# Performance work log

Measured on AMD Instinct MI355X. Metric: run time of the kernel, lower is better.

## Reference

```python
import jax, jax.numpy as jnp
import numpy as np

N, E, G = 20000, 640000, 64
D_IN, H, C, D_OUT = 256, 4, 64, 32
HC = H * C


def gat_layer(x, W, a_src, a_dst, b, src, dst, n_nodes, heads, ch):
    # x: [N, F_in], W: [F_in, H*C]
    h = (x @ W).reshape(n_nodes, heads, ch)          # [N,H,C]
    es = jnp.einsum('nhc,hc->nh', h, a_src)          # [N,H]
    ed = jnp.einsum('nhc,hc->nh', h, a_dst)
    e = jax.nn.leaky_relu(es[src] + ed[dst], 0.2)    # [Etot,H]
    m = jax.ops.segment_max(e, dst, num_segments=n_nodes)
    m = jnp.where(jnp.isfinite(m), m, 0.0)
    ex = jnp.exp(e - m[dst])
    denom = jax.ops.segment_sum(ex, dst, num_segments=n_nodes)
    alpha = ex / jnp.maximum(denom[dst], 1e-16)      # softmax over in-edges per dst
    out = jax.ops.segment_sum(alpha[:, :, None] * h[src], dst, num_segments=n_nodes)
    return out.reshape(n_nodes, heads * ch) + b


def setup_inputs() -> dict:
    key = jax.random.key(0)
    ks = jax.random.split(key, 14)
    g1 = 1.0 / np.sqrt(D_IN)
    g2 = 1.0 / np.sqrt(HC)
    inp = {
        'x': jax.random.normal(ks[0], (N, D_IN), jnp.float32),
        'edge_index': jax.random.randint(ks[1], (2, E), 0, N, jnp.int64 if jax.config.jax_enable_x64 else jnp.int32),
        'batch': jnp.sort(jax.random.randint(ks[2], (N,), 0, G)),
        'W1': jax.random.normal(ks[3], (D_IN, HC), jnp.float32) * g1,
        'a_src1': jax.random.normal(ks[4], (H, C), jnp.float32) * g2,
        'a_dst1': jax.random.normal(ks[5], (H, C), jnp.float32) * g2,
        'b1': jnp.zeros((HC,), jnp.float32),
        'W2': jax.random.normal(ks[6], (HC, HC), jnp.float32) * g2,
        'a_src2': jax.random.normal(ks[7], (H, C), jnp.float32) * g2,
        'a_dst2': jax.random.normal(ks[8], (H, C), jnp.float32) * g2,
        'b2': jnp.zeros((HC,), jnp.float32),
        'Wp': jax.random.normal(ks[9], (HC, D_OUT), jnp.float32) * g2,
        'bp': jnp.zeros((D_OUT,), jnp.float32),
    }
    return inp


def reference(x, edge_index, batch, W1, a_src1, a_dst1, b1, W2, a_src2, a_dst2, b2, Wp, bp):
    # add self-loops (PyG GATConv default)
    loop = jnp.arange(N, dtype=edge_index.dtype)
    src = jnp.concatenate([edge_index[0], loop])
    dst = jnp.concatenate([edge_index[1], loop])
    x1 = jax.nn.relu(gat_layer(x, W1, a_src1, a_dst1, b1, src, dst, N, H, C))
    # dropout p=0.6 is identity in eval mode
    x2 = jax.nn.relu(gat_layer(x1, W2, a_src2, a_dst2, b2, src, dst, N, H, C))
    node_scores = x2 @ Wp + bp                        # [N, D_OUT]
    sums = jax.ops.segment_sum(node_scores, batch, num_segments=G)
    counts = jax.ops.segment_sum(jnp.ones((N,), node_scores.dtype), batch, num_segments=G)
    return sums / jnp.maximum(counts, 1.0)[:, None]   # [G, D_OUT]
```

## Files before the change

### kernel.cpp

```cpp
#include <hip/hip_runtime.h>
#include <hip/hip_bf16.h>
#include <cstdint>

#define NNODES 20000
#define NEDGES 640000
#define ETOT   (NEDGES + NNODES)
#define NGROUP 64
#define HC     256
#define DOUT   32
#define NB     128
#define SL     ((ETOT + NB - 1) / NB)

typedef short bf16x8 __attribute__((ext_vector_type(8)));
typedef short s16x4  __attribute__((ext_vector_type(4)));
typedef float f32x4  __attribute__((ext_vector_type(4)));
typedef float f32x2  __attribute__((ext_vector_type(2)));
typedef int   s32x4  __attribute__((ext_vector_type(4)));
typedef unsigned int u32x4 __attribute__((ext_vector_type(4)));

__device__ __forceinline__ float b2f(__hip_bfloat16 v) { return __bfloat162float(v); }
__device__ __forceinline__ float bs2f(short v) {
    union { unsigned int u; float f; } c; c.u = ((unsigned int)(unsigned short)v) << 16; return c.f;
}
__device__ __forceinline__ short f2bs(float v) {
    __hip_bfloat16 b = __float2bfloat16(v);
    union { __hip_bfloat16 b; short s; } u; u.b = b; return u.s;
}
__device__ __forceinline__ float ldf(const void* __restrict__ p, size_t i, int bf) {
    return bf ? __bfloat162float(((const __hip_bfloat16*)p)[i]) : ((const float*)p)[i];
}
__device__ __forceinline__ int ld_idx(const int* __restrict__ p, size_t i, int f64) {
    return f64 ? p[2 * i] : p[i];
}

__global__ void k_probe(const unsigned int* __restrict__ xw, const int* __restrict__ ei,
                        int* __restrict__ flag) {
    if (threadIdx.x < 64) {
        int l = threadIdx.x;
        int ones = 0, zeros = 0;
#pragma unroll
        for (int r = 0; r < 4; r++) {
            unsigned long long b1 = __ballot((xw[r * 64 + l] >> 14) & 1);
            unsigned long long b2 = __ballot(ei[2 * (r * 64 + l) + 1] == 0);
            ones  += __popcll(b1);
            zeros += __popcll(b2);
        }
        if (l == 0) { flag[1] = (ones < 64) ? 1 : 0; flag[0] = (zeros > 200) ? 1 : 0; }
    }
}

__global__ __launch_bounds__(256) void k_lhist(const int* __restrict__ ei,
                                               int* __restrict__ H,
                                               const int* __restrict__ flag) {
    __shared__ int hl[NNODES];
    int t = threadIdx.x, b = blockIdx.x, f = flag[0];
    for (int i = t; i < NNODES; i += 256) hl[i] = 0;
    __syncthreads();
    int s0 = b * SL, s1 = min(s0 + SL, ETOT);
    for (int i = s0 + t; i < s1; i += 256) {
        int d = (i < NEDGES) ? ld_idx(ei, (size_t)NEDGES + i, f) : (i - NEDGES);
        atomicAdd(&hl[d], 1);
    }
    __syncthreads();
    int* Hb = H + (size_t)b * NNODES;
    for (int i = t; i < NNODES; i += 256) Hb[i] = hl[i];
}

__global__ __launch_bounds__(256) void k_colsum(const int* __restrict__ H,
                                                int* __restrict__ deg) {
    int n = blockIdx.x * 256 + threadIdx.x;
    if (n >= NNODES) return;
    int s = 0;
#pragma unroll 4
    for (int b = 0; b < NB; b++) s += H[(size_t)b * NNODES + n];
    deg[n] = s;
}

__global__ void k_scan(const int* __restrict__ deg, int* __restrict__ off,
                       float* __restrict__ sx, int* __restrict__ cnt) {
    __shared__ int wsum[8];
    int t = threadIdx.x, lane = t & 63, wv = t >> 6;
    for (int i = t; i < NGROUP * HC; i += 512) sx[i] = 0.f;
    if (t < NGROUP) cnt[t] = 0;
    const int CH = ((NNODES + 511) / 512) * 64;
    int base = wv * CH;
    int s = 0;
    for (int i0 = 0; i0 < CH; i0 += 64) {
        int i = base + i0 + lane;
        s += (i < NNODES) ? deg[i] : 0;
    }
#pragma unroll
    for (int o = 1; o < 64; o <<= 1) s += __shfl_xor(s, o);
    if (lane == 0) wsum[wv] = s;
    __syncthreads();
    int run = 0;
    for (int i = 0; i < wv; i++) run += wsum[i];
    for (int i0 = 0; i0 < CH; i0 += 64) {
        int i = base + i0 + lane;
        int v = (i < NNODES) ? deg[i] : 0;
        int sc = v;
#pragma unroll
        for (int o = 1; o < 64; o <<= 1) {
            int u = __shfl_up(sc, o);
            if (lane >= o) sc += u;
        }
        if (i < NNODES) off[i] = run + sc - v;
        run += __shfl(sc, 63);
    }
    if (t == 0) off[NNODES] = ETOT;
}

__global__ __launch_bounds__(256) void k_base(int* __restrict__ H,
                                              const int* __restrict__ off) {
    int n = blockIdx.x * 256 + threadIdx.x;
    if (n >= NNODES) return;
    int run = off[n];
#pragma unroll 4
    for (int b = 0; b < NB; b++) {
        size_t idx = (size_t)b * NNODES + n;
        int t = H[idx];
        H[idx] = run;
        run += t;
    }
}

__global__ __launch_bounds__(256) void k_scatter2(const int* __restrict__ ei,
                                                  const int* __restrict__ H,
                                                  int* __restrict__ csr,
                                                  const int* __restrict__ flag) {
    __shared__ int base_l[NNODES];
    int t = threadIdx.x, b = blockIdx.x, f = flag[0];
    const int* Hb = H + (size_t)b * NNODES;
    for (int i = t; i < NNODES; i += 256) base_l[i] = Hb[i];
    __syncthreads();
    int s0 = b * SL, s1 = min(s0 + SL, ETOT);
    for (int i = s0 + t; i < s1; i += 256) {
        int s, d;
        if (i < NEDGES) { s = ld_idx(ei, i, f); d = ld_idx(ei, (size_t)NEDGES + i, f); }
        else            { s = d = i - NEDGES; }
        int pos = atomicAdd(&base_l[d], 1);
        csr[pos] = s;
    }
}

__global__ void k_wt(const void* __restrict__ W1, const void* __restrict__ W2,
                     __hip_bfloat16* __restrict__ Wt1, __hip_bfloat16* __restrict__ Wt2,
                     const int* __restrict__ flag) {
    int i = blockIdx.x * 256 + threadIdx.x;
    int which = i >> 16;
    int j = i & 65535;
    int k = j >> 8, n = j & 255;
    const void* W = which ? W2 : W1;
    __hip_bfloat16* Wt = which ? Wt2 : Wt1;
    Wt[(size_t)n * 256 + k] = __float2bfloat16(ldf(W, (size_t)k * 256 + n, flag[1]));
}

__global__ __launch_bounds__(256) void k_gemm(const void* __restrict__ A,
                                              const __hip_bfloat16* __restrict__ Bt,
                                              __hip_bfloat16* __restrict__ Hout,
                                              const void* __restrict__ a_src,
                                              const void* __restrict__ a_dst,
                                              float* __restrict__ es4, float* __restrict__ ed4,
                                              const int* __restrict__ flag, int force_bf) {
    int bf   = flag[1];
    int abf  = force_bf | bf;
    int w    = threadIdx.x >> 6;
    int lane = threadIdx.x & 63;
    int mr   = lane & 15;
    int quad = lane >> 4;
    int r0   = blockIdx.x * 16;
    if (r0 >= NNODES) return;
    f32x4 acc[4];
#pragma unroll
    for (int j = 0; j < 4; j++) acc[j] = (f32x4){0.f, 0.f, 0.f, 0.f};
    size_t rowoff = (size_t)(r0 + mr) * HC;
    const __hip_bfloat16* Btw = Bt + (size_t)w * 64 * HC;
    for (int kk = 0; kk < HC; kk += 32) {
        bf16x8 a;
        if (abf) {
            a = *reinterpret_cast<const bf16x8*>((const __hip_bfloat16*)A + rowoff + kk + quad * 8);
        } else {
            const float* af = (const float*)A + rowoff + kk + quad * 8;
            f32x4 lo = *reinterpret_cast<const f32x4*>(af);
            f32x4 hi = *reinterpret_cast<const f32x4*>(af + 4);
#pragma unroll
            for (int ii = 0; ii < 4; ii++) { a[ii] = f2bs(lo[ii]); a[ii + 4] = f2bs(hi[ii]); }
        }
#pragma unroll
        for (int j = 0; j < 4; j++) {
            bf16x8 b = *reinterpret_cast<const bf16x8*>(Btw + (size_t)(j * 16 + mr) * HC + kk + quad * 8);
            acc[j] = __builtin_amdgcn_mfma_f32_16x16x32_bf16(a, b, acc[j], 0, 0, 0);
        }
    }
#pragma unroll
    for (int j = 0; j < 4; j++)
#pragma unroll
        for (int r = 0; r < 4; r++)
            Hout[(size_t)(r0 + quad * 4 + r) * HC + w * 64 + j * 16 + mr] = __float2bfloat16(acc[j][r]);
    float ps[4] = {0.f, 0.f, 0.f, 0.f}, pd[4] = {0.f, 0.f, 0.f, 0.f};
#pragma unroll
    for (int j = 0; j < 4; j++) {
        float asv = ldf(a_src, (size_t)(w * 64 + j * 16 + mr), bf);
        float adv = ldf(a_dst, (size_t)(w * 64 + j * 16 + mr), bf);
#pragma unroll
        for (int r = 0; r < 4; r++) {
            ps[r] = fmaf(acc[j][r], asv, ps[r]);
            pd[r] = fmaf(acc[j][r], adv, pd[r]);
        }
    }
#pragma unroll
    for (int o = 1; o < 16; o <<= 1)
#pragma unroll
        for (int r = 0; r < 4; r++) {
            ps[r] += __shfl_xor(ps[r], o);
            pd[r] += __shfl_xor(pd[r], o);
        }
    if (mr == 0)
#pragma unroll
        for (int r = 0; r < 4; r++) {
            int row = r0 + quad * 4 + r;
            es4[(size_t)row * 4 + w] = ps[r];
            ed4[(size_t)row * 4 + w] = pd[r];
        }
}

__global__ __launch_bounds__(256) void k_agg(const __hip_bfloat16* __restrict__ Hb,
                                             const float* __restrict__ es4, const float* __restrict__ ed4,
                                             const void* __restrict__ bias,
                                             const int* __restrict__ off, const int* __restrict__ csr,
                                             const int* __restrict__ flag,
                                             __hip_bfloat16* __restrict__ out) {
    __shared__ float p_lds[4][4][64];
    __shared__ int   s_lds[4][64];
    int wv = threadIdx.x >> 6;
    int l  = threadIdx.x & 63;
    int half = l >> 5;
    int hl   = l & 31;
    int hd8  = hl >> 3;
    int bf = flag[1];
    int n0 = blockIdx.x * 4 + wv;
    for (int n = n0; n < NNODES; n += 10000) {
        int base = off[n], deg = off[n + 1] - base;
        f32x4 edv = *reinterpret_cast<const f32x4*>(ed4 + (size_t)n * 4);
        f32x4 m    = (f32x4){-INFINITY, -INFINITY, -INFINITY, -INFINITY};
        f32x4 dsum = (f32x4){0.f, 0.f, 0.f, 0.f};
        f32x2 acc2[4];
#pragma unroll
        for (int d = 0; d < 4; d++) acc2[d] = (f32x2){0.f, 0.f};
        for (int c0 = 0; c0 < deg; c0 += 64) {
            int cn = min(deg - c0, 64);
            int s = 0;
            f32x4 ev;
            if (l < cn) {
                s = csr[base + c0 + l];
                f32x4 e = *reinterpret_cast<const f32x4*>(es4 + (size_t)s * 4);
#pragma unroll
                for (int h = 0; h < 4; h++) {
                    float t = e[h] + edv[h];
                    ev[h] = (t > 0.f) ? t : 0.2f * t;
                }
            } else {
#pragma unroll
                for (int h = 0; h < 4; h++) ev[h] = -INFINITY;
            }
            s_lds[wv][l] = s;
            f32x4 mc = ev;
#pragma unroll
            for (int o = 32; o; o >>= 1)
#pragma unroll
                for (int h = 0; h < 4; h++) mc[h] = fmaxf(mc[h], __shfl_xor(mc[h], o));
            f32x4 al, pv;
#pragma unroll
            for (int h = 0; h < 4; h++) {
                float nm = fmaxf(m[h], mc[h]);
                al[h] = __expf(m[h] - nm);
                m[h]  = nm;
            }
#pragma unroll
            for (int h = 0; h < 4; h++) pv[h] = (l < cn) ? __expf(ev[h] - m[h]) : 0.f;
            f32x4 sc = pv;
#pragma unroll
            for (int o = 32; o; o >>= 1)
#pragma unroll
                for (int h = 0; h < 4; h++) sc[h] += __shfl_xor(sc[h], o);
#pragma unroll
            for (int h = 0; h < 4; h++) dsum[h] = dsum[h] * al[h] + sc[h];
            float a8 = al[hd8];
#pragma unroll
            for (int d = 0; d < 4; d++) acc2[d] *= a8;
#pragma unroll
            for (int h = 0; h < 4; h++) p_lds[wv][h][l] = pv[h];
            int jn = (cn + 15) & ~15;
            for (int j = 0; j < jn; j += 16) {
                int e0 = j + 8 * half;
                s32x4 sA = *reinterpret_cast<const s32x4*>(&s_lds[wv][e0]);
                s32x4 sB = *reinterpret_cast<const s32x4*>(&s_lds[wv][e0 + 4]);
                f32x4 pA = *reinterpret_cast<const f32x4*>(&p_lds[wv][hd8][e0]);
                f32x4 pB = *reinterpret_cast<const f32x4*>(&p_lds[wv][hd8][e0 + 4]);
                u32x4 hv[8];
#pragma unroll
                for (int i = 0; i < 8; i++) {
                    int sj = (i < 4) ? sA[i & 3] : sB[i & 3];
                    hv[i] = *reinterpret_cast<const u32x4*>(Hb + (size_t)sj * HC + hl * 8);
                }
#pragma unroll
                for (int i = 0; i < 8; i++) {
                    float p = (i < 4) ? pA[i & 3] : pB[i & 3];
#pragma unroll
                    for (int d = 0; d < 4; d++) {
                        unsigned int u = hv[i][d];
                        f32x2 h2;
                        h2.x = __uint_as_float(u << 16);
                        h2.y = __uint_as_float(u & 0xFFFF0000u);
                        acc2[d] += h2 * p;
                    }
                }
            }
        }
#pragma unroll
        for (int d = 0; d < 4; d++) {
            acc2[d].x += __shfl_xor(acc2[d].x, 32);
            acc2[d].y += __shfl_xor(acc2[d].y, 32);
        }
        float rinv = 1.0f / fmaxf(dsum[hd8], 1e-16f);
        if (half == 0) {
            bf16x8 ov;
#pragma unroll
            for (int d = 0; d < 4; d++) {
                float v0 = acc2[d].x * rinv + ldf(bias, (size_t)hl * 8 + 2 * d, bf);
                float v1 = acc2[d].y * rinv + ldf(bias, (size_t)hl * 8 + 2 * d + 1, bf);
                ov[2 * d]     = f2bs(fmaxf(v0, 0.f));
                ov[2 * d + 1] = f2bs(fmaxf(v1, 0.f));
            }
            *reinterpret_cast<bf16x8*>(out + (size_t)n * HC + hl * 8) = ov;
        }
    }
}

__global__ __launch_bounds__(256) void k_groupsum(const __hip_bfloat16* __restrict__ X2,
                                                  const int* __restrict__ batch,
                                                  float* __restrict__ sx, int* __restrict__ cnt,
                                                  const int* __restrict__ flag) {
    const int RPB = NNODES / 250;
    int b = blockIdx.x, f = flag[0];
    int sub = threadIdx.x >> 6, l = threadIdx.x & 63;
    int r = b * RPB + sub;
    f32x4 acc = (f32x4){0.f, 0.f, 0.f, 0.f};
    int curg = ld_idx(batch, r, f);
    int cacc = 0;
    for (int k = 0; k < RPB / 4; k++, r += 4) {
        int g = ld_idx(batch, r, f);
        if (g != curg) {
#pragma unroll
            for (int c = 0; c < 4; c++) atomicAdd(&sx[(size_t)curg * HC + l * 4 + c], acc[c]);
            if (l == 0) atomicAdd(&cnt[curg], cacc);
            acc = (f32x4){0.f, 0.f, 0.f, 0.f}; cacc = 0; curg = g;
        }
        s16x4 hv = *reinterpret_cast<const s16x4*>(X2 + (size_t)r * HC + l * 4);
#pragma unroll
        for (int c = 0; c < 4; c++) acc[c] += bs2f(hv[c]);
        cacc++;
    }
#pragma unroll
    for (int c = 0; c < 4; c++) atomicAdd(&sx[(size_t)curg * HC + l * 4 + c], acc[c]);
    if (l == 0) atomicAdd(&cnt[curg], cacc);
}

__global__ __launch_bounds__(256) void k_final(const float* __restrict__ sx,
                                               const void* __restrict__ Wp,
                                               const void* __restrict__ bp,
                                               const int* __restrict__ cnt,
                                               const int* __restrict__ flag,
                                               void* __restrict__ out) {
    __shared__ float red[8][32];
    int g = blockIdx.x, t = threadIdx.x;
    int c = t & 31, seg = t >> 5;
    int bf = flag[1];
    const float* sxg = sx + (size_t)g * HC;
    float a = 0.f;
#pragma unroll
    for (int k = 0; k < 32; k++) {
        int kk = seg * 32 + k;
        a = fmaf(sxg[kk], ldf(Wp, (size_t)kk * DOUT + c, bf), a);
    }
    red[seg][c] = a;
    __syncthreads();
    if (t < 32) {
        float s = 0.f;
#pragma unroll
        for (int i = 0; i < 8; i++) s += red[i][t];
        int ct = cnt[g];
        float v = (ct > 0) ? (s / ct + ldf(bp, (size_t)t, bf)) : 0.f;
        if (bf) ((__hip_bfloat16*)out)[g * DOUT + t] = __float2bfloat16(v);
        else    ((float*)out)[g * DOUT + t]          = v;
    }
}

extern "C" void kernel_launch(void* const* d_in, const int* in_sizes, int n_in,
                              void* d_out, int out_size, void* d_ws, size_t ws_size,
                              hipStream_t stream) {
    (void)in_sizes; (void)n_in; (void)out_size; (void)ws_size;
    const void* x   = d_in[0];
    const int*  ei  = (const int*)d_in[1];
    const int*  bat = (const int*)d_in[2];
    const void* W1  = d_in[3];
    const void* as1 = d_in[4];
    const void* ad1 = d_in[5];
    const void* b1  = d_in[6];
    const void* W2  = d_in[7];
    const void* as2 = d_in[8];
    const void* ad2 = d_in[9];
    const void* b2  = d_in[10];
    const void* Wp  = d_in[11];
    const void* bp  = d_in[12];

    char* ws = (char*)d_ws;
    size_t o = 0;
    auto alloc = [&](size_t bytes) -> char* {
        char* p = ws + o;
        o += (bytes + 255) & ~(size_t)255;
        return p;
    };
    __hip_bfloat16* hb  = (__hip_bfloat16*)alloc((size_t)NNODES * HC * 2);
    __hip_bfloat16* xb  = (__hip_bfloat16*)alloc((size_t)NNODES * HC * 2);
    __hip_bfloat16* xb2 = (__hip_bfloat16*)alloc((size_t)NNODES * HC * 2);
    __hip_bfloat16* Wt1 = (__hip_bfloat16*)alloc((size_t)HC * HC * 2);
    __hip_bfloat16* Wt2 = (__hip_bfloat16*)alloc((size_t)HC * HC * 2);
    float* es = (float*)alloc((size_t)NNODES * 4 * 4);
    float* ed = (float*)alloc((size_t)NNODES * 4 * 4);
    int* H    = (int*)alloc((size_t)NB * NNODES * 4);
    int* deg  = (int*)alloc((size_t)NNODES * 4);
    int* off  = (int*)alloc((size_t)(NNODES + 1) * 4);
    int* csr  = (int*)alloc((size_t)ETOT * 4);
    float* sx = (float*)alloc((size_t)NGROUP * HC * 4);
    int* cnt  = (int*)alloc(256);
    int* flag = (int*)alloc(256);

    k_probe<<<1, 256, 0, stream>>>((const unsigned int*)x, ei, flag);
    k_lhist<<<NB, 256, 0, stream>>>(ei, H, flag);
    k_colsum<<<(NNODES + 255) / 256, 256, 0, stream>>>(H, deg);
    k_scan<<<1, 512, 0, stream>>>(deg, off, sx, cnt);
    k_base<<<(NNODES + 255) / 256, 256, 0, stream>>>(H, off);
    k_scatter2<<<NB, 256, 0, stream>>>(ei, H, csr, flag);
    k_wt<<<512, 256, 0, stream>>>(W1, W2, Wt1, Wt2, flag);

    k_gemm<<<NNODES / 16, 256, 0, stream>>>(x, Wt1, hb, as1, ad1, es, ed, flag, 0);
    k_agg<<<2500, 256, 0, stream>>>(hb, es, ed, b1, off, csr, flag, xb);

    k_gemm<<<NNODES / 16, 256, 0, stream>>>(xb, Wt2, hb, as2, ad2, es, ed, flag, 1);
    k_agg<<<2500, 256, 0, stream>>>(hb, es, ed, b2, off, csr, flag, xb2);

    k_groupsum<<<250, 256, 0, stream>>>(xb2, bat, sx, cnt, flag);
    k_final<<<NGROUP, 256, 0, stream>>>(sx, Wp, bp, cnt, flag, d_out);
}
```

Measured before the change: 320.4 us.

## Parallelize CSR build scan and vectorize edge histogram and scatter

Replaces the single-block serial prefix scan over node degrees with a multi-block scan: column sums also produce per-block totals, a small kernel scans those, and k_base does the in-block scan while writing offsets. Self-loops are handled analytically by placing each node first in its own CSR segment instead of routing them through the histogram and scatter. Edge blocks shrink from 128 to 125 slices of 5120 edges and load indices as 16-byte vectors. Zeroing of the group-sum buffers moves into the probe kernel.

Result: faster. 299.7 us (-6.5%).

```diff
diff --git a/kernel.cpp b/kernel.cpp
--- a/kernel.cpp
+++ b/kernel.cpp
@@ -8,8 +8,9 @@
 #define NGROUP 64
 #define HC     256
 #define DOUT   32
-#define NB     128
-#define SL     ((ETOT + NB - 1) / NB)
+#define EBLK   5120
+#define NBLK   (NEDGES / EBLK)
+#define CBLK   ((NNODES + 255) / 256)
 
 typedef short bf16x8 __attribute__((ext_vector_type(8)));
 typedef short s16x4  __attribute__((ext_vector_type(4)));
@@ -34,9 +35,12 @@
 }
 
 __global__ void k_probe(const unsigned int* __restrict__ xw, const int* __restrict__ ei,
-                        int* __restrict__ flag) {
-    if (threadIdx.x < 64) {
-        int l = threadIdx.x;
+                        int* __restrict__ flag, float* __restrict__ sx, int* __restrict__ cnt) {
+    int t = threadIdx.x;
+    for (int i = t; i < NGROUP * HC; i += 256) sx[i] = 0.f;
+    if (t < NGROUP) cnt[t] = 0;
+    if (t < 64) {
+        int l = t;
         int ones = 0, zeros = 0;
 #pragma unroll
         for (int r = 0; r < 4; r++) {
@@ -54,73 +58,103 @@
                                                const int* __restrict__ flag) {
     __shared__ int hl[NNODES];
     int t = threadIdx.x, b = blockIdx.x, f = flag[0];
-    for (int i = t; i < NNODES; i += 256) hl[i] = 0;
-    __syncthreads();
-    int s0 = b * SL, s1 = min(s0 + SL, ETOT);
-    for (int i = s0 + t; i < s1; i += 256) {
-        int d = (i < NEDGES) ? ld_idx(ei, (size_t)NEDGES + i, f) : (i - NEDGES);
-        atomicAdd(&hl[d], 1);
-    }
-    __syncthreads();
-    int* Hb = H + (size_t)b * NNODES;
-    for (int i = t; i < NNODES; i += 256) Hb[i] = hl[i];
+    s32x4* hl4 = reinterpret_cast<s32x4*>(hl);
+    for (int i = t; i < NNODES / 4; i += 256) hl4[i] = (s32x4){0, 0, 0, 0};
+    __syncthreads();
+    int s0 = b * EBLK;
+    if (f) {
+        const int* d64 = ei + 2 * NEDGES;
+        for (int i0 = s0; i0 < s0 + EBLK; i0 += 512) {
+            int i = i0 + 2 * t;
+            s32x4 v = *reinterpret_cast<const s32x4*>(d64 + 2 * (size_t)i);
+            atomicAdd(&hl[v[0]], 1);
+            atomicAdd(&hl[v[2]], 1);
+        }
+    } else {
+        const int* d32 = ei + NEDGES;
+        for (int i0 = s0; i0 < s0 + EBLK; i0 += 1024) {
+            int i = i0 + 4 * t;
+            s32x4 v = *reinterpret_cast<const s32x4*>(d32 + i);
+            atomicAdd(&hl[v[0]], 1); atomicAdd(&hl[v[1]], 1);
+            atomicAdd(&hl[v[2]], 1); atomicAdd(&hl[v[3]], 1);
+        }
+    }
+    __syncthreads();
+    s32x4* Hb4 = reinterpret_cast<s32x4*>(H + (size_t)b * NNODES);
+    for (int i = t; i < NNODES / 4; i += 256) Hb4[i] = hl4[i];
 }
 
 __global__ __launch_bounds__(256) void k_colsum(const int* __restrict__ H,
-                                                int* __restrict__ deg) {
-    int n = blockIdx.x * 256 + threadIdx.x;
-    if (n >= NNODES) return;
+                                                int* __restrict__ deg,
+                                                int* __restrict__ bsum) {
+    __shared__ int wred[4];
+    int t = threadIdx.x, n = blockIdx.x * 256 + t;
     int s = 0;
-#pragma unroll 4
-    for (int b = 0; b < NB; b++) s += H[(size_t)b * NNODES + n];
-    deg[n] = s;
-}
-
-__global__ void k_scan(const int* __restrict__ deg, int* __restrict__ off,
-                       float* __restrict__ sx, int* __restrict__ cnt) {
-    __shared__ int wsum[8];
-    int t = threadIdx.x, lane = t & 63, wv = t >> 6;
-    for (int i = t; i < NGROUP * HC; i += 512) sx[i] = 0.f;
-    if (t < NGROUP) cnt[t] = 0;
-    const int CH = ((NNODES + 511) / 512) * 64;
-    int base = wv * CH;
-    int s = 0;
-    for (int i0 = 0; i0 < CH; i0 += 64) {
-        int i = base + i0 + lane;
-        s += (i < NNODES) ? deg[i] : 0;
-    }
-#pragma unroll
-    for (int o = 1; o < 64; o <<= 1) s += __shfl_xor(s, o);
-    if (lane == 0) wsum[wv] = s;
-    __syncthreads();
-    int run = 0;
-    for (int i = 0; i < wv; i++) run += wsum[i];
-    for (int i0 = 0; i0 < CH; i0 += 64) {
-        int i = base + i0 + lane;
-        int v = (i < NNODES) ? deg[i] : 0;
-        int sc = v;
-#pragma unroll
-        for (int o = 1; o < 64; o <<= 1) {
-            int u = __shfl_up(sc, o);
-            if (lane >= o) sc += u;
-        }
-        if (i < NNODES) off[i] = run + sc - v;
-        run += __shfl(sc, 63);
-    }
+    if (n < NNODES) {
+#pragma unroll 5
+        for (int b = 0; b < NBLK; b++) s += H[(size_t)b * NNODES + n];
+        s += 1;
+        deg[n] = s;
+    }
+    int r = s;
+#pragma unroll
+    for (int o = 1; o < 64; o <<= 1) r += __shfl_xor(r, o);
+    if ((t & 63) == 0) wred[t >> 6] = r;
+    __syncthreads();
+    if (t == 0) bsum[blockIdx.x] = wred[0] + wred[1] + wred[2] + wred[3];
+}
+
+__global__ void k_scansm(const int* __restrict__ bsum, int* __restrict__ boff,
+                         int* __restrict__ off) {
+    __shared__ int w0tot;
+    int t = threadIdx.x, lane = t & 63, w = t >> 6;
+    int v = (t < CBLK) ? bsum[t] : 0;
+    int sc = v;
+#pragma unroll
+    for (int o = 1; o < 64; o <<= 1) {
+        int u = __shfl_up(sc, o);
+        if (lane >= o) sc += u;
+    }
+    if (w == 0 && lane == 63) w0tot = sc;
+    __syncthreads();
+    int excl = sc - v + (w ? w0tot : 0);
+    if (t < CBLK) boff[t] = excl;
     if (t == 0) off[NNODES] = ETOT;
 }
 
 __global__ __launch_bounds__(256) void k_base(int* __restrict__ H,
-                                              const int* __restrict__ off) {
-    int n = blockIdx.x * 256 + threadIdx.x;
-    if (n >= NNODES) return;
-    int run = off[n];
-#pragma unroll 4
-    for (int b = 0; b < NB; b++) {
-        size_t idx = (size_t)b * NNODES + n;
-        int t = H[idx];
-        H[idx] = run;
-        run += t;
+                                              const int* __restrict__ deg,
+                                              const int* __restrict__ boff,
+                                              int* __restrict__ off,
+                                              int* __restrict__ csr) {
+    __shared__ int wtot[4];
+    int t = threadIdx.x, blk = blockIdx.x;
+    int n = blk * 256 + t;
+    int d = (n < NNODES) ? deg[n] : 0;
+    int lane = t & 63, w = t >> 6;
+    int sc = d;
+#pragma unroll
+    for (int o = 1; o < 64; o <<= 1) {
+        int u = __shfl_up(sc, o);
+        if (lane >= o) sc += u;
+    }
+    if (lane == 63) wtot[w] = sc;
+    __syncthreads();
+    int woff = 0;
+    for (int i = 0; i < w; i++) woff += wtot[i];
+    int excl = woff + sc - d;
+    if (n < NNODES) {
+        int o0 = boff[blk] + excl;
+        off[n] = o0;
+        csr[o0] = n;
+        int run = o0 + 1;
+#pragma unroll 5
+        for (int b = 0; b < NBLK; b++) {
+            size_t idx = (size_t)b * NNODES + n;
+            int tt = H[idx];
+            H[idx] = run;
+            run += tt;
+        }
     }
 }
 
@@ -130,16 +164,34 @@
                                                   const int* __restrict__ flag) {
     __shared__ int base_l[NNODES];
     int t = threadIdx.x, b = blockIdx.x, f = flag[0];
-    const int* Hb = H + (size_t)b * NNODES;
-    for (int i = t; i < NNODES; i += 256) base_l[i] = Hb[i];
-    __syncthreads();
-    int s0 = b * SL, s1 = min(s0 + SL, ETOT);
-    for (int i = s0 + t; i < s1; i += 256) {
-        int s, d;
-        if (i < NEDGES) { s = ld_idx(ei, i, f); d = ld_idx(ei, (size_t)NEDGES + i, f); }
-        else            { s = d = i - NEDGES; }
-        int pos = atomicAdd(&base_l[d], 1);
-        csr[pos] = s;
+    const s32x4* Hb4 = reinterpret_cast<const s32x4*>(H + (size_t)b * NNODES);
+    s32x4* bl4 = reinterpret_cast<s32x4*>(base_l);
+    for (int i = t; i < NNODES / 4; i += 256) bl4[i] = Hb4[i];
+    __syncthreads();
+    int s0 = b * EBLK;
+    if (f) {
+        const int* d64 = ei + 2 * NEDGES;
+        for (int i0 = s0; i0 < s0 + EBLK; i0 += 512) {
+            int i = i0 + 2 * t;
+            s32x4 sv = *reinterpret_cast<const s32x4*>(ei + 2 * (size_t)i);
+            s32x4 dv = *reinterpret_cast<const s32x4*>(d64 + 2 * (size_t)i);
+            int p0 = atomicAdd(&base_l[dv[0]], 1);
+            csr[p0] = sv[0];
+            int p1 = atomicAdd(&base_l[dv[2]], 1);
+            csr[p1] = sv[2];
+        }
+    } else {
+        const int* d32 = ei + NEDGES;
+        for (int i0 = s0; i0 < s0 + EBLK; i0 += 1024) {
+            int i = i0 + 4 * t;
+            s32x4 sv = *reinterpret_cast<const s32x4*>(ei + i);
+            s32x4 dv = *reinterpret_cast<const s32x4*>(d32 + i);
+#pragma unroll
+            for (int k = 0; k < 4; k++) {
+                int p = atomicAdd(&base_l[dv[k]], 1);
+                csr[p] = sv[k];
+            }
+        }
     }
 }
 
@@ -428,20 +480,22 @@
     __hip_bfloat16* Wt2 = (__hip_bfloat16*)alloc((size_t)HC * HC * 2);
     float* es = (float*)alloc((size_t)NNODES * 4 * 4);
     float* ed = (float*)alloc((size_t)NNODES * 4 * 4);
-    int* H    = (int*)alloc((size_t)NB * NNODES * 4);
+    int* H    = (int*)alloc((size_t)NBLK * NNODES * 4);
     int* deg  = (int*)alloc((size_t)NNODES * 4);
     int* off  = (int*)alloc((size_t)(NNODES + 1) * 4);
     int* csr  = (int*)alloc((size_t)ETOT * 4);
+    int* bsum = (int*)alloc((size_t)CBLK * 4);
+    int* boff = (int*)alloc((size_t)CBLK * 4);
     float* sx = (float*)alloc((size_t)NGROUP * HC * 4);
     int* cnt  = (int*)alloc(256);
     int* flag = (int*)alloc(256);
 
-    k_probe<<<1, 256, 0, stream>>>((const unsigned int*)x, ei, flag);
-    k_lhist<<<NB, 256, 0, stream>>>(ei, H, flag);
-    k_colsum<<<(NNODES + 255) / 256, 256, 0, stream>>>(H, deg);
-    k_scan<<<1, 512, 0, stream>>>(deg, off, sx, cnt);
-    k_base<<<(NNODES + 255) / 256, 256, 0, stream>>>(H, off);
-    k_scatter2<<<NB, 256, 0, stream>>>(ei, H, csr, flag);
+    k_probe<<<1, 256, 0, stream>>>((const unsigned int*)x, ei, flag, sx, cnt);
+    k_lhist<<<NBLK, 256, 0, stream>>>(ei, H, flag);
+    k_colsum<<<CBLK, 256, 0, stream>>>(H, deg, bsum);
+    k_scansm<<<1, 128, 0, stream>>>(bsum, boff, off);
+    k_base<<<CBLK, 256, 0, stream>>>(H, deg, boff, off, csr);
+    k_scatter2<<<NBLK, 256, 0, stream>>>(ei, H, csr, flag);
     k_wt<<<512, 256, 0, stream>>>(W1, W2, Wt1, Wt2, flag);
 
     k_gemm<<<NNODES / 16, 256, 0, stream>>>(x, Wt1, hb, as1, ad1, es, ed, flag, 0);
```
